# Kernel tuning notes

Measured on AMD Instinct MI355X. Metric: run time of the kernel, lower is better.

The kernel has to match this reference:

```python
import jax, jax.numpy as jnp
import numpy as np

MD = 4            # max_displacement
DP = 1            # dilation_patch
PATCH = 2 * MD + 1  # 9
# kernel_size=1, stride=1, padding=0, dilation=1 -> oH=H, oW=W


def setup_inputs() -> dict:
    key = jax.random.key(0)
    k1, k2 = jax.random.split(key)
    N, C, H, W = 8, 256, 128, 128
    input1 = jax.random.normal(k1, (N, C, H, W), dtype=jnp.float32)
    input2 = jax.random.normal(k2, (N, C, H, W), dtype=jnp.float32)
    return {"input1": input1, "input2": input2}


def _correlation(input1, input2):
    # out[n, py, px, y, x] = sum_c input1[n,c,y,x] * input2[n,c, y+(py-MD)*DP, x+(px-MD)*DP]
    # with zero padding for out-of-bounds input2 positions (mmcv semantics, no
    # normalization by channel count).
    N, C, H, W = input1.shape
    pad = MD * DP
    x2 = jnp.pad(input2, ((0, 0), (0, 0), (pad, pad), (pad, pad)))
    rows = []
    for py in range(PATCH):  # small fixed displacement grid (9x9)
        cols = []
        for px in range(PATCH):
            sh, sw = py * DP, px * DP
            x2s = x2[:, :, sh:sh + H, sw:sw + W]  # shifted input2, [N,C,H,W]
            cols.append(jnp.einsum('nchw,nchw->nhw', input1, x2s))
        rows.append(jnp.stack(cols, axis=1))  # [N, PATCH, H, W]
    return jnp.stack(rows, axis=1)  # [N, PATCH, PATCH, H, W]


def reference(input1, input2):
    return _correlation(input1, input2)
```

## Files before the change

### kernel.cpp

```cpp
#include <hip/hip_runtime.h>
#include <hip/hip_bf16.h>

typedef __attribute__((ext_vector_type(8))) short short8v;
typedef __attribute__((ext_vector_type(4))) float f32x4;

#define H_  128
#define W_  128
#define C_  256
#define HW_ 16384

#define MFMA32(a, b, c) __builtin_amdgcn_mfma_f32_16x16x32_bf16(a, b, c, 0, 0, 0)

__device__ __forceinline__ short bf16b(float f) {
    unsigned u = __float_as_uint(f);
    u += 0x7fffu + ((u >> 16) & 1u);
    return (short)(u >> 16);
}

__global__ __launch_bounds__(512, 2)
void corr_kernel(const float* __restrict__ in1, const float* __restrict__ in2,
                 float* __restrict__ out)
{
    __shared__ short lds2[2][24 * 4 * 32 * 8];
    __shared__ float ldso[9 * 257];

    const int tid  = threadIdx.x;
    const int lane = tid & 63;
    const int wid  = tid >> 6;
    const int m    = lane & 15;
    const int g    = lane >> 4;

    int bid = blockIdx.x;
    int swz = (bid & 7) * 64 + (bid >> 3);
    int n   = swz >> 6;
    int h0  = ((swz >> 3) & 7) << 4;
    int w0  = (swz & 7) << 4;

    const float* in1n = in1 + (size_t)n * (C_ * HW_);
    const float* in2n = in2 + (size_t)n * (C_ * HW_);

    int  lwoff[5]; long gbase[5]; bool act[5], inb[5];
#pragma unroll
    for (int s = 0; s < 5; ++s) {
        int u  = tid + s * 512;
        act[s] = (u < 2304);
        int c  = u % 24;
        int rj = u / 24;
        int j  = rj & 3;
        int r  = rj >> 2;
        int row = h0 - 4 + r;
        int col = w0 - 4 + c;
        inb[s] = act[s] && ((unsigned)row < 128u) && ((unsigned)col < 128u);
        gbase[s] = inb[s] ? ((long)(j * 8) * HW_ + (long)row * W_ + col) : 0;
        lwoff[s] = ((r * 4 + j) * 32 + c) * 8;
    }
    const long abase = (long)(8 * g) * HW_ + (long)(h0 + 2 * wid) * W_ + (w0 + m);

    {
        short8v z = (short8v)0;
        short8v* zp = (short8v*)&lds2[0][0];
#pragma unroll
        for (int i = 0; i < 12; ++i) zp[tid + i * 512] = z;
    }
    __syncthreads();
    __builtin_amdgcn_sched_barrier(0);

    f32x4 acc[2][9][2];
#pragma unroll
    for (int a = 0; a < 2; ++a)
#pragma unroll
        for (int d = 0; d < 9; ++d)
#pragma unroll
            for (int t = 0; t < 2; ++t)
                acc[a][d][t] = (f32x4){0.f, 0.f, 0.f, 0.f};

    {
        float sf[5][8];
#pragma unroll
        for (int s = 0; s < 5; ++s)
            if (act[s])
#pragma unroll
                for (int i = 0; i < 8; ++i) {
                    float v = in2n[gbase[s] + (long)i * HW_];
                    sf[s][i] = inb[s] ? v : 0.f;
                }
#pragma unroll
        for (int s = 0; s < 5; ++s)
            if (act[s]) {
                short8v v8;
#pragma unroll
                for (int i = 0; i < 8; ++i) v8[i] = bf16b(sf[s][i]);
                *(short8v*)&lds2[0][lwoff[s]] = v8;
            }
    }

#pragma unroll 1
    for (int t = 0; t < 8; ++t) {
        __syncthreads();
        __builtin_amdgcn_sched_barrier(0);
        const int rb = t & 1;

        float af[2][8];
#pragma unroll
        for (int rs = 0; rs < 2; ++rs)
#pragma unroll
            for (int i = 0; i < 8; ++i)
                af[rs][i] = in1n[abase + (long)(32 * t + i) * HW_ + rs * W_];

        float sf[5][8];
        if (t < 7) {
            const long koff = (long)((t + 1) * 32) * HW_;
#pragma unroll
            for (int s = 0; s < 5; ++s)
                if (act[s])
#pragma unroll
                    for (int i = 0; i < 8; ++i) {
                        float v = in2n[gbase[s] + koff + (long)i * HW_];
                        sf[s][i] = inb[s] ? v : 0.f;
                    }
        }

        short8v a8[2];
#pragma unroll
        for (int rs = 0; rs < 2; ++rs)
#pragma unroll
            for (int i = 0; i < 8; ++i) a8[rs][i] = bf16b(af[rs][i]);

        const short* lb = &lds2[rb][0];
#pragma unroll
        for (int dy = 0; dy < 9; ++dy) {
#pragma unroll
            for (int rs = 0; rs < 2; ++rs) {
                int r = 2 * wid + rs + dy;
                int ro = (r * 4 + g) * 256;
#pragma unroll
                for (int nt = 0; nt < 2; ++nt) {
                    short8v b = *(const short8v*)&lb[ro + (nt * 16 + m) * 8];
                    acc[rs][dy][nt] = MFMA32(a8[rs], b, acc[rs][dy][nt]);
                }
            }
        }

        if (t < 7) {
#pragma unroll
            for (int s = 0; s < 5; ++s)
                if (act[s]) {
                    short8v v8;
#pragma unroll
                    for (int i = 0; i < 8; ++i) v8[i] = bf16b(sf[s][i]);
                    *(short8v*)&lds2[rb ^ 1][lwoff[s]] = v8;
                }
        }
    }

    const size_t outb = (size_t)n * 81 * HW_;
#pragma unroll
    for (int dy = 0; dy < 9; ++dy) {
        __syncthreads();
        __builtin_amdgcn_sched_barrier(0);
#pragma unroll
        for (int rs = 0; rs < 2; ++rs) {
            int hl = 2 * wid + rs;
#pragma unroll
            for (int nt = 0; nt < 2; ++nt) {
#pragma unroll
                for (int i = 0; i < 4; ++i) {
                    int mm = 4 * g + i;
                    int dx = nt * 16 + m - mm;
                    if (dx >= 0 && dx < 9)
                        ldso[dx * 257 + hl * 16 + mm] = acc[rs][dy][nt][i];
                }
            }
        }
        __syncthreads();
        __builtin_amdgcn_sched_barrier(0);
#pragma unroll
        for (int e = 0; e < 5; ++e) {
            int t = tid + e * 512;
            if (t < 2304) {
                int dx  = t >> 8;
                int rem = t & 255;
                out[outb + (size_t)(dy * 9 + dx) * HW_ +
                    (size_t)(h0 + (rem >> 4)) * W_ + (w0 + (rem & 15))] = ldso[dx * 257 + rem];
            }
        }
    }
}

extern "C" void kernel_launch(void* const* d_in, const int* in_sizes, int n_in,
                              void* d_out, int out_size, void* d_ws, size_t ws_size,
                              hipStream_t stream) {
    const float* in1 = (const float*)d_in[0];
    const float* in2 = (const float*)d_in[1];
    float* out = (float*)d_out;
    corr_kernel<<<dim3(512), dim3(512), 0, stream>>>(in1, in2, out);
}
```

Baseline: 106.2 us.

## Load input2 halo with float4 vector loads and share LDS B-fragments across rows

The input2 halo staging now has each thread load four contiguous columns with one 16-byte load instead of eight scalar strided loads. The bf16 values are scattered into the same channel-interleaved LDS layout with 2-byte stores. The MFMA loop loads each LDS row once and feeds it to both accumulator row-sets, cutting B-fragment LDS reads from 36 to 20 per step. Offsets switch to 32-bit ints to save address arithmetic. The cost is many more narrow LDS stores with possible bank conflicts, plus halo boundary handling at 4-column granularity.

```diff
diff --git a/kernel.cpp b/kernel.cpp
--- a/kernel.cpp
+++ b/kernel.cpp
@@ -1,7 +1,9 @@
 #include <hip/hip_runtime.h>
 #include <hip/hip_bf16.h>
+#include <limits.h>
 
 typedef __attribute__((ext_vector_type(8))) short short8v;
+typedef __attribute__((ext_vector_type(4))) short short4v;
 typedef __attribute__((ext_vector_type(4))) float f32x4;
 
 #define H_  128
@@ -39,22 +41,23 @@
     const float* in1n = in1 + (size_t)n * (C_ * HW_);
     const float* in2n = in2 + (size_t)n * (C_ * HW_);
 
-    int  lwoff[5]; long gbase[5]; bool act[5], inb[5];
+    int lwoff[9]; int gofs[9];
 #pragma unroll
-    for (int s = 0; s < 5; ++s) {
-        int u  = tid + s * 512;
-        act[s] = (u < 2304);
-        int c  = u % 24;
-        int rj = u / 24;
-        int j  = rj & 3;
-        int r  = rj >> 2;
-        int row = h0 - 4 + r;
-        int col = w0 - 4 + c;
-        inb[s] = act[s] && ((unsigned)row < 128u) && ((unsigned)col < 128u);
-        gbase[s] = inb[s] ? ((long)(j * 8) * HW_ + (long)row * W_ + col) : 0;
-        lwoff[s] = ((r * 4 + j) * 32 + c) * 8;
+    for (int s = 0; s < 9; ++s) {
+        int u    = tid + s * 512;
+        int q    = u % 6;
+        int rest = u / 6;
+        int i    = rest & 7;
+        int rj   = rest >> 3;
+        int j    = rj & 3;
+        int r    = rj >> 2;
+        int row  = h0 - 4 + r;
+        int col0 = w0 - 4 + 4 * q;
+        bool inb = ((unsigned)row < 128u) && ((unsigned)col0 < 125u);
+        gofs[s]  = inb ? ((j * 8 + i) * HW_ + row * W_ + col0) : INT_MIN;
+        lwoff[s] = ((r * 4 + j) * 32 + 4 * q) * 8 + i;
     }
-    const long abase = (long)(8 * g) * HW_ + (long)(h0 + 2 * wid) * W_ + (w0 + m);
+    const int abase = (8 * g) * HW_ + (h0 + 2 * wid) * W_ + (w0 + m);
 
     {
         short8v z = (short8v)0;
@@ -75,23 +78,19 @@
                 acc[a][d][t] = (f32x4){0.f, 0.f, 0.f, 0.f};
 
     {
-        float sf[5][8];
+        f32x4 sv[9];
 #pragma unroll
-        for (int s = 0; s < 5; ++s)
-            if (act[s])
+        for (int s = 0; s < 9; ++s) {
+            f32x4 v = (f32x4){0.f, 0.f, 0.f, 0.f};
+            if (gofs[s] != INT_MIN) v = *(const f32x4*)(in2n + gofs[s]);
+            sv[s] = v;
+        }
 #pragma unroll
-                for (int i = 0; i < 8; ++i) {
-                    float v = in2n[gbase[s] + (long)i * HW_];
-                    sf[s][i] = inb[s] ? v : 0.f;
-                }
+        for (int s = 0; s < 9; ++s) {
+            short* p = &lds2[0][lwoff[s]];
 #pragma unroll
-        for (int s = 0; s < 5; ++s)
-            if (act[s]) {
-                short8v v8;
-#pragma unroll
-                for (int i = 0; i < 8; ++i) v8[i] = bf16b(sf[s][i]);
-                *(short8v*)&lds2[0][lwoff[s]] = v8;
-            }
+            for (int d = 0; d < 4; ++d) p[8 * d] = bf16b(sv[s][d]);
+        }
     }
 
 #pragma unroll 1
@@ -105,19 +104,17 @@
         for (int rs = 0; rs < 2; ++rs)
 #pragma unroll
             for (int i = 0; i < 8; ++i)
-                af[rs][i] = in1n[abase + (long)(32 * t + i) * HW_ + rs * W_];
+                af[rs][i] = in1n[abase + (32 * t + i) * HW_ + rs * W_];
 
-        float sf[5][8];
+        f32x4 sv[9];
         if (t < 7) {
-            const long koff = (long)((t + 1) * 32) * HW_;
+            const int koff = (t + 1) * 32 * HW_;
 #pragma unroll
-            for (int s = 0; s < 5; ++s)
-                if (act[s])
-#pragma unroll
-                    for (int i = 0; i < 8; ++i) {
-                        float v = in2n[gbase[s] + koff + (long)i * HW_];
-                        sf[s][i] = inb[s] ? v : 0.f;
-                    }
+            for (int s = 0; s < 9; ++s) {
+                f32x4 v = (f32x4){0.f, 0.f, 0.f, 0.f};
+                if (gofs[s] != INT_MIN) v = *(const f32x4*)(in2n + gofs[s] + koff);
+                sv[s] = v;
+            }
         }
 
         short8v a8[2];
@@ -128,28 +125,27 @@
 
         const short* lb = &lds2[rb][0];
 #pragma unroll
-        for (int dy = 0; dy < 9; ++dy) {
-#pragma unroll
-            for (int rs = 0; rs < 2; ++rs) {
-                int r = 2 * wid + rs + dy;
-                int ro = (r * 4 + g) * 256;
-#pragma unroll
-                for (int nt = 0; nt < 2; ++nt) {
-                    short8v b = *(const short8v*)&lb[ro + (nt * 16 + m) * 8];
-                    acc[rs][dy][nt] = MFMA32(a8[rs], b, acc[rs][dy][nt]);
-                }
+        for (int rr = 0; rr < 10; ++rr) {
+            int ro = (((2 * wid + rr) * 4 + g) * 32) * 8;
+            short8v b0 = *(const short8v*)&lb[ro + m * 8];
+            short8v b1 = *(const short8v*)&lb[ro + (16 + m) * 8];
+            if (rr <= 8) {
+                acc[0][rr][0] = MFMA32(a8[0], b0, acc[0][rr][0]);
+                acc[0][rr][1] = MFMA32(a8[0], b1, acc[0][rr][1]);
+            }
+            if (rr >= 1) {
+                acc[1][rr - 1][0] = MFMA32(a8[1], b0, acc[1][rr - 1][0]);
+                acc[1][rr - 1][1] = MFMA32(a8[1], b1, acc[1][rr - 1][1]);
             }
         }
 
         if (t < 7) {
 #pragma unroll
-            for (int s = 0; s < 5; ++s)
-                if (act[s]) {
-                    short8v v8;
+            for (int s = 0; s < 9; ++s) {
+                short* p = &lds2[rb ^ 1][lwoff[s]];
 #pragma unroll
-                    for (int i = 0; i < 8; ++i) v8[i] = bf16b(sf[s][i]);
-                    *(short8v*)&lds2[rb ^ 1][lwoff[s]] = v8;
-                }
+                for (int d = 0; d < 4; ++d) p[8 * d] = bf16b(sv[s][d]);
+            }
         }
     }
 
```

Measured after the change: 98.69 us. -7.1%, faster.
